# Kernel tuning notes

Hardware: AMD Instinct MI355X
Metric: run time of the kernel (lower is better)

The kernel has to match this reference:

```python
import jax, jax.numpy as jnp
import numpy as np

TEMP = 0.07
GAMMA1 = 0.8
GAMMA2 = 0.8
TAU = 0.1
BETA = 40.0
NUM_CT = 5
EPS = float(np.finfo(np.float32).eps)


def setup_inputs() -> dict:
    key = jax.random.key(0)
    ks = jax.random.split(key, 12)
    B, D, N, Bc = 8192, 512, 1000000, 4096
    img = jax.random.normal(ks[0], (B, D), jnp.float32)
    txt = jax.random.normal(ks[1], (B, D), jnp.float32)
    # CLIP-style unit-norm features keep sim in [-1,1] so exp() stays stable
    img = img / jnp.linalg.norm(img, axis=1, keepdims=True)
    txt = txt / jnp.linalg.norm(txt, axis=1, keepdims=True)
    image_ids = jax.random.randint(ks[2], (B,), 0, N)
    text_ids = jax.random.randint(ks[3], (B,), 0, N)
    slabel = jax.random.randint(ks[4], (B,), 0, 2)
    img_feas_c = jax.random.normal(ks[5], (Bc, D), jnp.float32)
    img_feas_c = img_feas_c / jnp.linalg.norm(img_feas_c, axis=1, keepdims=True)
    txt_feas_c = jax.random.normal(ks[6], (NUM_CT, D), jnp.float32)
    txt_feas_c = txt_feas_c / jnp.linalg.norm(txt_feas_c, axis=1, keepdims=True)
    labels_c = jax.random.randint(ks[7], (Bc,), 0, NUM_CT)
    last_loss_c = jax.random.uniform(ks[8], (Bc,), jnp.float32) * 2.0
    # persistent moving-average buffers (positive values, as they hold past exp-means)
    s_I = jax.random.uniform(ks[9], (N,), jnp.float32) + 0.5
    s_T = jax.random.uniform(ks[10], (N,), jnp.float32) + 0.5
    u = jnp.zeros((NUM_CT,), jnp.float32)
    return dict(image_features=img, text_features=txt, image_ids=image_ids,
                text_ids=text_ids, slabel=slabel, epoch=1,
                img_feas_c=img_feas_c, txt_feas_c=txt_feas_c, labels_c=labels_c,
                last_loss_c=last_loss_c, s_I=s_I, s_T=s_T, u=u)


def reference(image_features, text_features, image_ids, text_ids, slabel, epoch,
              img_feas_c, txt_feas_c, labels_c, last_loss_c, s_I, s_T, u):
    sg = jax.lax.stop_gradient
    # pairwise similarity GEMM  [B, B]
    sim = jnp.einsum('id,jd->ij', image_features, text_features)
    diag = jnp.diagonal(sim)
    pos = slabel == 1
    neg = ~pos
    pos_image_ids = image_ids[pos]
    pos_text_ids = text_ids[pos]
    # masked pairwise similarity differences: [P, B-P] and [B-P, P]
    image_diffs = (sim - diag[:, None])[pos][:, neg]
    text_diffs = (sim - diag[None, :])[neg][:, pos]
    image_diffs_d = sg(image_diffs / TEMP)
    text_diffs_d = sg(text_diffs / TEMP)
    exp_i = jnp.exp(image_diffs_d)
    exp_t = jnp.exp(text_diffs_d)
    g_I = jnp.mean(exp_i, axis=1, keepdims=True)   # [P, 1]
    g_T = jnp.mean(exp_t, axis=0, keepdims=True)   # [1, P]
    if epoch == 0:
        sI = g_I
        sT = g_T
    else:
        sI = ((1.0 - GAMMA1) * s_I[pos_image_ids] + GAMMA1 * g_I.squeeze()).reshape(g_I.shape)
        sT = ((1.0 - GAMMA1) * s_T[pos_text_ids] + GAMMA1 * g_T.squeeze()).reshape(g_T.shape)
    # persistent buffer scatter updates
    s_I_new = s_I.at[pos_image_ids].set(sI.squeeze())
    s_T_new = s_T.at[pos_text_ids].set(sT.squeeze())
    w_i = exp_i / (sI + EPS)
    w_t = exp_t / (sT + EPS)
    image_loss = jnp.mean(w_i * image_diffs, axis=1)
    text_loss = jnp.mean(w_t * text_diffs, axis=0)
    contrastive_loss = image_loss.mean() + text_loss.mean()
    # per-class CE penalty branch
    logits = (1.0 / TAU) * img_feas_c @ txt_feas_c.T           # [Bc, NUM_CT]
    logp = jax.nn.log_softmax(logits, axis=-1)
    ce = -logp[jnp.arange(logits.shape[0]), labels_c]          # [Bc]
    counts = jax.ops.segment_sum(jnp.ones_like(ce), labels_c, num_segments=NUM_CT)
    present = counts > 0
    safe_counts = jnp.maximum(counts, 1.0)
    mean_by_cls = jax.ops.segment_sum(ce, labels_c, num_segments=NUM_CT) / safe_counts
    mean_by_cls_last = jax.ops.segment_sum(last_loss_c, labels_c, num_segments=NUM_CT) / safe_counts
    cv = mean_by_cls - mean_by_cls_last
    u_sum = jnp.sum(jnp.where(present, u, 0.0))
    u_upd = jnp.where(u_sum == 0.0, sg(cv), (1.0 - GAMMA2) * u + GAMMA2 * sg(cv))
    u_new = jnp.where(present, u_upd, u)
    beta = BETA  # cosine=False
    cl = sg(jnp.maximum(beta * u_new, 0.0)) * mean_by_cls * TAU
    n_present = jnp.sum(present.astype(jnp.float32))
    constraint_mean = jnp.sum(jnp.where(present, cl, 0.0)) / n_present
    loss = contrastive_loss + constraint_mean
    return loss, s_I_new, s_T_new, u_new
```

## Files before the change

### kernel.cpp

```cpp
#include <hip/hip_runtime.h>

#define NBATCH 8192
#define DD 512
#define NIDS 1000000
#define BCNT 4096
#define NCT 5
#define INV_TEMP 14.285714285714286f
#define EPSF 1.1920929e-07f

typedef __attribute__((ext_vector_type(8))) short bf16x8;
typedef __attribute__((ext_vector_type(4))) float f32x4;
typedef __attribute__((ext_vector_type(8))) unsigned short u16x8;

#define OFF_LP     ((size_t)0)
#define OFF_CE1    ((size_t)1024)
#define OFF_CE2    ((size_t)2304)
#define OFF_CE3    ((size_t)3584)
#define OFF_POS    ((size_t)(32*1024))
#define OFF_RNK    ((size_t)(64*1024))
#define OFF_CNT    ((size_t)(96*1024))
#define OFF_DA     ((size_t)(100*1024))
#define OFF_RA0    ((size_t)(132*1024))
#define OFF_RB0    ((size_t)(164*1024))
#define OFF_RA1    ((size_t)(196*1024))
#define OFF_RB1    ((size_t)(228*1024))
#define OFF_SIV    ((size_t)(260*1024))
#define OFF_STV    ((size_t)(292*1024))
#define OFF_WINI   ((size_t)(324*1024))
#define OFF_WINT   (OFF_WINI + 4000000)
#define OFF_MA     (OFF_WINT + 4000000)
#define MATB       ((size_t)(8192*512*2))
#define OFF_MB     (OFF_MA + MATB)
#define OFF_MC     (OFF_MB + MATB)
#define OFF_MD     (OFF_MC + MATB)


__device__ __forceinline__ unsigned short f2bf(float x) {
    unsigned int u = __float_as_uint(x);
    unsigned int r = (u + 0x7fffu + ((u >> 16) & 1u)) >> 16;
    return (unsigned short)r;
}

__global__ __launch_bounds__(256) void k_pre(
        const float* __restrict__ sI, const float* __restrict__ sT,
        float* __restrict__ out, int* __restrict__ winI, int* __restrict__ winT,
        float* __restrict__ rA0, float* __restrict__ rB0,
        float* __restrict__ rA1, float* __restrict__ rB1,
        const int* __restrict__ slabel, int* __restrict__ pos,
        int* __restrict__ rnk, int* __restrict__ cnts,
        const float* __restrict__ imgc, const float* __restrict__ tfc,
        const int* __restrict__ labels, const float* __restrict__ lastl,
        float* __restrict__ ce1, float* __restrict__ ce2, float* __restrict__ ce3) {
    int bid = blockIdx.x;
    int tid = threadIdx.x;
    int iv = bid * 256 + tid;
    if (iv < NIDS) {
        out[1 + iv] = sI[iv];
        out[1 + NIDS + iv] = sT[iv];
        winI[iv] = -1;
        winT[iv] = -1;
    }
    if (iv < NBATCH) { rA0[iv] = 0.f; rB0[iv] = 0.f; rA1[iv] = 0.f; rB1[iv] = 0.f; }
    if (bid < 3907) return;

    if (bid == 3971) {
        __shared__ int sums[256];
        int base = tid * 32;
        int c = 0;
        for (int j = 0; j < 32; ++j) c += (slabel[base + j] == 1);
        sums[tid] = c;
        __syncthreads();
        for (int off = 1; off < 256; off <<= 1) {
            int add = (tid >= off) ? sums[tid - off] : 0;
            __syncthreads();
            sums[tid] += add;
            __syncthreads();
        }
        int p = sums[tid] - c;
        for (int j = 0; j < 32; ++j) {
            int idx = base + j;
            if (slabel[idx] == 1) { pos[p] = idx; rnk[idx] = p; p++; }
            else rnk[idx] = idx - p;
        }
        if (tid == 255) { cnts[0] = sums[255]; cnts[1] = NBATCH - sums[255]; }
    } else {
        int cb = bid - 3907;
        __shared__ float tS[NCT * DD];
        __shared__ float sce[NCT], scn[NCT], sls[NCT];
        for (int j = tid; j < NCT * DD; j += 256) tS[j] = tfc[j];
        if (tid < NCT) { sce[tid] = 0.f; scn[tid] = 0.f; sls[tid] = 0.f; }
        __syncthreads();
        int lane = tid & 63;
        int wid = tid >> 6;
        for (int it = 0; it < 16; ++it) {
            int r = it * 256 + cb * 4 + wid;
            const float4* ip = (const float4*)(imgc + (size_t)r * DD) + lane * 2;
            float4 a0 = ip[0], a1 = ip[1];
            float p[NCT];
#pragma unroll
            for (int c = 0; c < NCT; ++c) {
                const float* t = &tS[c * DD + lane * 8];
                p[c] = a0.x * t[0] + a0.y * t[1] + a0.z * t[2] + a0.w * t[3]
                     + a1.x * t[4] + a1.y * t[5] + a1.z * t[6] + a1.w * t[7];
            }
#pragma unroll
            for (int c = 0; c < NCT; ++c)
                for (int off = 32; off; off >>= 1) p[c] += __shfl_xor(p[c], off);
            if (lane == 0) {
                float l[NCT];
                float mx = -1e30f;
#pragma unroll
                for (int c = 0; c < NCT; ++c) { l[c] = p[c] * 10.0f; mx = fmaxf(mx, l[c]); }
                float ssum = 0.f;
#pragma unroll
                for (int c = 0; c < NCT; ++c) ssum += __expf(l[c] - mx);
                float lse = mx + __logf(ssum);
                int lb = labels[r];
                float ce = lse - l[lb];
                atomicAdd(&sce[lb], ce);
                atomicAdd(&scn[lb], 1.f);
                atomicAdd(&sls[lb], lastl[r]);
            }
        }
        __syncthreads();
        if (tid < NCT) {
            ce1[cb * 5 + tid] = sce[tid];
            ce2[cb * 5 + tid] = scn[tid];
            ce3[cb * 5 + tid] = sls[tid];
        }
    }
}

__global__ __launch_bounds__(256) void k_gather(
        const float* __restrict__ img, const float* __restrict__ txt,
        const int* __restrict__ slabel, const int* __restrict__ rnk,
        unsigned short* __restrict__ mA, unsigned short* __restrict__ mB,
        unsigned short* __restrict__ mC, unsigned short* __restrict__ mD,
        float* __restrict__ dA) {
    int tid = threadIdx.x;
    int i = blockIdx.x * 4 + (tid >> 6);
    int g = tid & 63;
    const float4* ip = (const float4*)(img + (size_t)i * DD) + g * 2;
    const float4* tp = (const float4*)(txt + (size_t)i * DD) + g * 2;
    float4 v0 = ip[0], v1 = ip[1], t0 = tp[0], t1 = tp[1];
    float part = v0.x * t0.x + v0.y * t0.y + v0.z * t0.z + v0.w * t0.w
               + v1.x * t1.x + v1.y * t1.y + v1.z * t1.z + v1.w * t1.w;
    for (int off = 32; off; off >>= 1) part += __shfl_xor(part, off);

    int lab = (slabel[i] == 1);
    int r = rnk[i];
    u16x8 oi, ot;
    oi[0] = f2bf(v0.x); oi[1] = f2bf(v0.y); oi[2] = f2bf(v0.z); oi[3] = f2bf(v0.w);
    oi[4] = f2bf(v1.x); oi[5] = f2bf(v1.y); oi[6] = f2bf(v1.z); oi[7] = f2bf(v1.w);
    ot[0] = f2bf(t0.x); ot[1] = f2bf(t0.y); ot[2] = f2bf(t0.z); ot[3] = f2bf(t0.w);
    ot[4] = f2bf(t1.x); ot[5] = f2bf(t1.y); ot[6] = f2bf(t1.z); ot[7] = f2bf(t1.w);

    int kc = g >> 2, gg = g & 3, rl = r & 127;
    int kb = (gg * 16) ^ ((rl & 6) << 3);
    size_t off = (size_t)(r >> 7) * 65536 + (size_t)kc * 4096 + rl * 32 + (kb >> 1);
    unsigned short* dI = lab ? mA : mD;
    unsigned short* dT = lab ? mC : mB;
    *(u16x8*)(dI + off) = oi;
    *(u16x8*)(dT + off) = ot;
    if (lab && g == 0) dA[r] = part;
}

__device__ __forceinline__ void gl16(const unsigned short* src, unsigned short* lds) {
    __builtin_amdgcn_global_load_lds((const __attribute__((address_space(1))) void*)src,
                                     (__attribute__((address_space(3))) void*)lds, 16, 0, 0);
}

#define VM4()  asm volatile("s_waitcnt vmcnt(4)" ::: "memory")
#define VM0()  asm volatile("s_waitcnt vmcnt(0)" ::: "memory")
#define BARR() asm volatile("s_barrier" ::: "memory")

__global__ __launch_bounds__(256) void k_gemm(
        const unsigned short* __restrict__ mA, const unsigned short* __restrict__ mB,
        const unsigned short* __restrict__ mC, const unsigned short* __restrict__ mD,
        const float* __restrict__ dA, const int* __restrict__ cnts,
        float* __restrict__ rA0, float* __restrict__ rB0,
        float* __restrict__ rA1, float* __restrict__ rB1) {
    int P = cnts[0], Nn = cnts[1];
    int bm = blockIdx.x * 128, bn = blockIdx.y * 128;
    if (bm >= P || bn >= Nn) return;
    int z = blockIdx.z;
    const unsigned short* Ap = (z ? mC : mA) + (size_t)blockIdx.x * 65536;
    const unsigned short* Bp = (z ? mD : mB) + (size_t)blockIdx.y * 65536;
    float* rA = z ? rA1 : rA0;
    float* rB = z ? rB1 : rB0;

    __shared__ __align__(16) char SRAW[36864];
    unsigned short* S0 = (unsigned short*)SRAW;

    int tid = threadIdx.x;
    int lane = tid & 63;
    int wid = tid >> 6;
    int wr = wid >> 1, wc = wid & 1;
    int soff = tid * 8;

    int kswz = ((lane >> 4) * 16) ^ ((lane & 6) << 3);
    int abyte = (wr * 64 + (lane & 15)) * 64 + kswz;
    int bbyte = (wc * 64 + (lane & 15)) * 64 + kswz;

    f32x4 acc[4][4];
#pragma unroll
    for (int m = 0; m < 4; ++m)
#pragma unroll
        for (int n = 0; n < 4; ++n) acc[m][n] = (f32x4){0.f, 0.f, 0.f, 0.f};

#define STAGE(kt, p) do { \
        gl16(Ap + (kt) * 4096 + soff,        S0 + (p) * 8192 + soff); \
        gl16(Ap + (kt) * 4096 + soff + 2048, S0 + (p) * 8192 + soff + 2048); \
        gl16(Bp + (kt) * 4096 + soff,        S0 + (p) * 8192 + 4096 + soff); \
        gl16(Bp + (kt) * 4096 + soff + 2048, S0 + (p) * 8192 + 4096 + soff + 2048); } while (0)

    STAGE(0, 0);
    STAGE(1, 1);
    VM4();
    BARR();

#pragma unroll
    for (int kt = 0; kt < 16; ++kt) {
        const int cur = kt & 1;
        bf16x8 af[4], bfv[4];
#pragma unroll
        for (int m = 0; m < 4; ++m)
            af[m] = *(const bf16x8*)((const char*)S0 + cur * 16384 + abyte + m * 1024);
#pragma unroll
        for (int n = 0; n < 4; ++n)
            bfv[n] = *(const bf16x8*)((const char*)S0 + cur * 16384 + 8192 + bbyte + n * 1024);
#pragma unroll
        for (int m = 0; m < 4; ++m)
#pragma unroll
            for (int n = 0; n < 4; ++n)
                acc[m][n] = __builtin_amdgcn_mfma_f32_16x16x32_bf16(af[m], bfv[n], acc[m][n], 0, 0, 0);
        if (kt < 15) {
            BARR();
            if (kt + 2 < 16) {
                STAGE(kt + 2, cur);
                VM4();
            } else {
                VM0();
            }
            BARR();
        }
    }
#undef STAGE

    BARR();
    float* F = (float*)SRAW;
    int col = lane & 15;
    int rsub = (lane >> 4) * 4;
    int rowbase = bm + wr * 64;
    int colb = bn + wc * 64 + col;
    int fb = ((wc << 7) + (wr << 6)) * 36 + col * 2;
#pragma unroll
    for (int m = 0; m < 4; ++m) {
#pragma unroll
        for (int r = 0; r < 4; ++r) {
            int wrow = m * 16 + rsub + r;
            float dv = dA[rowbase + wrow];
            float pa = 0.f, pb = 0.f;
#pragma unroll
            for (int n = 0; n < 4; ++n) {
                int gcol = colb + n * 16;
                float sv = acc[m][n][r];
                float df = sv - dv;
                float e = (gcol < Nn) ? __expf(df * INV_TEMP) : 0.f;
                pa += e;
                pb += e * df;
            }
            *(float2*)&F[fb + wrow * 36] = make_float2(pa, pb);
        }
    }
    BARR();
    {
        int row = tid >> 1;
        int half = tid & 1;
        const float4* Fr = (const float4*)&F[((half << 7) + row) * 36];
        float sa = 0.f, sb = 0.f;
#pragma unroll
        for (int q = 0; q < 8; ++q) {
            float4 v = Fr[q];
            sa += v.x + v.z;
            sb += v.y + v.w;
        }
        sa += __shfl_xor(sa, 1);
        sb += __shfl_xor(sb, 1);
        int grow = bm + row;
        if (!half && grow < P) {
            atomicAdd(&rA[grow], sa);
            atomicAdd(&rB[grow], sb);
        }
    }
}

__global__ void k_posfin(const int* __restrict__ cnts, const int* __restrict__ pos,
                         const float* __restrict__ rA0, const float* __restrict__ rB0,
                         const float* __restrict__ rA1, const float* __restrict__ rB1,
                         const int* __restrict__ image_ids, const int* __restrict__ text_ids,
                         const float* __restrict__ sIin, const float* __restrict__ sTin,
                         const int* __restrict__ epochp,
                         float* __restrict__ sIv, float* __restrict__ sTv,
                         int* __restrict__ winI, int* __restrict__ winT,
                         float* __restrict__ lp) {
    int k = blockIdx.x * 256 + threadIdx.x;
    int P = cnts[0], Nn = cnts[1];
    float invNn = 1.f / (float)Nn;
    int epoch = epochp[0];
    float lI = 0.f, lT = 0.f;
    if (k < P) {
        int i = pos[k];
        int idI = image_ids[i], idT = text_ids[i];
        float gI = rA0[k] * invNn;
        float sIvk = (epoch == 0) ? gI : 0.2f * sIin[idI] + 0.8f * gI;
        lI = (rB0[k] * invNn) / (sIvk + EPSF);
        float gT = rA1[k] * invNn;
        float sTvk = (epoch == 0) ? gT : 0.2f * sTin[idT] + 0.8f * gT;
        lT = (rB1[k] * invNn) / (sTvk + EPSF);
        sIv[k] = sIvk;
        sTv[k] = sTvk;
        atomicMax(&winI[idI], k);
        atomicMax(&winT[idT], k);
    }
    for (int off = 32; off; off >>= 1) { lI += __shfl_xor(lI, off); lT += __shfl_xor(lT, off); }
    if ((threadIdx.x & 63) == 0) {
        int slot = blockIdx.x * 4 + (threadIdx.x >> 6);
        lp[slot * 2] = lI;
        lp[slot * 2 + 1] = lT;
    }
}

__global__ void k_fin(const int* __restrict__ cnts, const int* __restrict__ pos,
                      const int* __restrict__ image_ids, const int* __restrict__ text_ids,
                      const int* __restrict__ winI, const int* __restrict__ winT,
                      const float* __restrict__ sIv, const float* __restrict__ sTv,
                      const float* __restrict__ lp, const float* __restrict__ ce1,
                      const float* __restrict__ ce2, const float* __restrict__ ce3,
                      const float* __restrict__ u, float* __restrict__ out) {
    int P = cnts[0];
    int k = blockIdx.x * 256 + threadIdx.x;
    if (k < P) {
        int i = pos[k];
        int a = image_ids[i];
        if (winI[a] == k) out[1 + a] = sIv[k];
        int b = text_ids[i];
        if (winT[b] == k) out[1 + NIDS + b] = sTv[k];
    }
    if (blockIdx.x == 0 && threadIdx.x < 64) {
        int lane = threadIdx.x;
        float lI = lp[2 * lane] + lp[2 * (lane + 64)];
        float lT = lp[2 * lane + 1] + lp[2 * (lane + 64) + 1];
        for (int off = 32; off; off >>= 1) { lI += __shfl_xor(lI, off); lT += __shfl_xor(lT, off); }
        float ce[NCT], cn[NCT], ls[NCT];
#pragma unroll
        for (int c = 0; c < NCT; ++c) {
            float a1 = ce1[lane * 5 + c], a2 = ce2[lane * 5 + c], a3 = ce3[lane * 5 + c];
            for (int off = 32; off; off >>= 1) {
                a1 += __shfl_xor(a1, off);
                a2 += __shfl_xor(a2, off);
                a3 += __shfl_xor(a3, off);
            }
            ce[c] = a1; cn[c] = a2; ls[c] = a3;
        }
        if (lane == 0) {
            float Pf = (float)P;
            float contrast = lI / Pf + lT / Pf;
            float u_sum = 0.f;
            float mc[NCT], cv[NCT], u_new[NCT];
            bool pres[NCT];
#pragma unroll
            for (int c = 0; c < NCT; ++c) {
                pres[c] = cn[c] > 0.f;
                float safe = fmaxf(cn[c], 1.f);
                mc[c] = ce[c] / safe;
                float ml = ls[c] / safe;
                cv[c] = mc[c] - ml;
                if (pres[c]) u_sum += u[c];
            }
            float np_ = 0.f, csum = 0.f;
#pragma unroll
            for (int c = 0; c < NCT; ++c) {
                float uu = (u_sum == 0.f) ? cv[c] : 0.2f * u[c] + 0.8f * cv[c];
                u_new[c] = pres[c] ? uu : u[c];
                if (pres[c]) {
                    np_ += 1.f;
                    csum += fmaxf(40.0f * u_new[c], 0.f) * mc[c] * 0.1f;
                }
                out[1 + 2 * NIDS + c] = u_new[c];
            }
            out[0] = contrast + csum / np_;
        }
    }
}

extern "C" void kernel_launch(void* const* d_in, const int* in_sizes, int n_in,
                              void* d_out, int out_size, void* d_ws, size_t ws_size,
                              hipStream_t stream) {
    const float* img = (const float*)d_in[0];
    const float* txt = (const float*)d_in[1];
    const int* image_ids = (const int*)d_in[2];
    const int* text_ids = (const int*)d_in[3];
    const int* slabel = (const int*)d_in[4];
    const int* epoch = (const int*)d_in[5];
    const float* imgc = (const float*)d_in[6];
    const float* tfc = (const float*)d_in[7];
    const int* labels = (const int*)d_in[8];
    const float* lastl = (const float*)d_in[9];
    const float* sI = (const float*)d_in[10];
    const float* sT = (const float*)d_in[11];
    const float* u = (const float*)d_in[12];
    float* out = (float*)d_out;
    char* ws = (char*)d_ws;

    float* lp = (float*)(ws + OFF_LP);
    float* ce1 = (float*)(ws + OFF_CE1);
    float* ce2 = (float*)(ws + OFF_CE2);
    float* ce3 = (float*)(ws + OFF_CE3);
    int* pos = (int*)(ws + OFF_POS);
    int* rnk = (int*)(ws + OFF_RNK);
    int* cnts = (int*)(ws + OFF_CNT);
    float* dA = (float*)(ws + OFF_DA);
    float* rA0 = (float*)(ws + OFF_RA0);
    float* rB0 = (float*)(ws + OFF_RB0);
    float* rA1 = (float*)(ws + OFF_RA1);
    float* rB1 = (float*)(ws + OFF_RB1);
    float* sIv = (float*)(ws + OFF_SIV);
    float* sTv = (float*)(ws + OFF_STV);
    int* winI = (int*)(ws + OFF_WINI);
    int* winT = (int*)(ws + OFF_WINT);
    unsigned short* mA = (unsigned short*)(ws + OFF_MA);
    unsigned short* mB = (unsigned short*)(ws + OFF_MB);
    unsigned short* mC = (unsigned short*)(ws + OFF_MC);
    unsigned short* mD = (unsigned short*)(ws + OFF_MD);

    k_pre<<<3972, 256, 0, stream>>>(sI, sT, out, winI, winT, rA0, rB0, rA1, rB1,
                                    slabel, pos, rnk, cnts,
                                    imgc, tfc, labels, lastl, ce1, ce2, ce3);
    k_gather<<<2048, 256, 0, stream>>>(img, txt, slabel, rnk, mA, mB, mC, mD, dA);
    k_gemm<<<dim3(64, 64, 2), 256, 0, stream>>>(mA, mB, mC, mD, dA, cnts, rA0, rB0, rA1, rB1);
    k_posfin<<<32, 256, 0, stream>>>(cnts, pos, rA0, rB0, rA1, rB1, image_ids, text_ids,
                                     sI, sT, epoch, sIv, sTv, winI, winT, lp);
    k_fin<<<32, 256, 0, stream>>>(cnts, pos, image_ids, text_ids, winI, winT,
                                  sIv, sTv, lp, ce1, ce2, ce3, u, out);
}
```

Before: 87.98 us.

## Widen GEMM block tile to 128x256 so each A tile is reused across two B tiles

The similarity GEMM block tile grows from 128x128 to 128x256. Each block now stages one A panel and two B panels per k-step, each wave computes a 64x128 sub-tile (32 accumulators), and the grid halves in y. The aim is to cut redundant A loads and LDS traffic per MFMA and to amortize barriers. In exchange it doubles the accumulator registers, raises LDS use to 48KB, and halves the number of blocks, which may reduce occupancy or leave some CUs idle.

After: 92.73 us. 5.4% more time.

```diff
diff --git a/kernel.cpp b/kernel.cpp
--- a/kernel.cpp
+++ b/kernel.cpp
@@ -170,26 +170,29 @@
                                      (__attribute__((address_space(3))) void*)lds, 16, 0, 0);
 }
 
-#define VM4()  asm volatile("s_waitcnt vmcnt(4)" ::: "memory")
+#define VM6()  asm volatile("s_waitcnt vmcnt(6)" ::: "memory")
 #define VM0()  asm volatile("s_waitcnt vmcnt(0)" ::: "memory")
+#define LGK0() asm volatile("s_waitcnt lgkmcnt(0)" ::: "memory")
 #define BARR() asm volatile("s_barrier" ::: "memory")
 
-__global__ __launch_bounds__(256) void k_gemm(
+__global__ __launch_bounds__(256, 2) void k_gemm(
         const unsigned short* __restrict__ mA, const unsigned short* __restrict__ mB,
         const unsigned short* __restrict__ mC, const unsigned short* __restrict__ mD,
         const float* __restrict__ dA, const int* __restrict__ cnts,
         float* __restrict__ rA0, float* __restrict__ rB0,
         float* __restrict__ rA1, float* __restrict__ rB1) {
     int P = cnts[0], Nn = cnts[1];
-    int bm = blockIdx.x * 128, bn = blockIdx.y * 128;
+    int bm = blockIdx.x * 128, bn = blockIdx.y * 256;
     if (bm >= P || bn >= Nn) return;
     int z = blockIdx.z;
     const unsigned short* Ap = (z ? mC : mA) + (size_t)blockIdx.x * 65536;
-    const unsigned short* Bp = (z ? mD : mB) + (size_t)blockIdx.y * 65536;
+    const unsigned short* Bp0 = (z ? mD : mB) + (size_t)(blockIdx.y * 2) * 65536;
+    const unsigned short* Bp1 = Bp0 + 65536;
+
     float* rA = z ? rA1 : rA0;
     float* rB = z ? rB1 : rB0;
 
-    __shared__ __align__(16) char SRAW[36864];
+    __shared__ __align__(16) char SRAW[49152];
     unsigned short* S0 = (unsigned short*)SRAW;
 
     int tid = threadIdx.x;
@@ -200,45 +203,57 @@
 
     int kswz = ((lane >> 4) * 16) ^ ((lane & 6) << 3);
     int abyte = (wr * 64 + (lane & 15)) * 64 + kswz;
-    int bbyte = (wc * 64 + (lane & 15)) * 64 + kswz;
-
-    f32x4 acc[4][4];
+    int bbyte = (lane & 15) * 64 + kswz;
+    int bregion = 8192 + wc * 8192;
+
+    f32x4 acc[4][8];
 #pragma unroll
     for (int m = 0; m < 4; ++m)
 #pragma unroll
-        for (int n = 0; n < 4; ++n) acc[m][n] = (f32x4){0.f, 0.f, 0.f, 0.f};
+        for (int n = 0; n < 8; ++n) acc[m][n] = (f32x4){0.f, 0.f, 0.f, 0.f};
 
 #define STAGE(kt, p) do { \
-        gl16(Ap + (kt) * 4096 + soff,        S0 + (p) * 8192 + soff); \
-        gl16(Ap + (kt) * 4096 + soff + 2048, S0 + (p) * 8192 + soff + 2048); \
-        gl16(Bp + (kt) * 4096 + soff,        S0 + (p) * 8192 + 4096 + soff); \
-        gl16(Bp + (kt) * 4096 + soff + 2048, S0 + (p) * 8192 + 4096 + soff + 2048); } while (0)
+        gl16(Ap + (kt) * 4096 + soff,         S0 + (p) * 12288 + soff); \
+        gl16(Ap + (kt) * 4096 + soff + 2048,  S0 + (p) * 12288 + soff + 2048); \
+        gl16(Bp0 + (kt) * 4096 + soff,        S0 + (p) * 12288 + 4096 + soff); \
+        gl16(Bp0 + (kt) * 4096 + soff + 2048, S0 + (p) * 12288 + 4096 + soff + 2048); \
+        gl16(Bp1 + (kt) * 4096 + soff,        S0 + (p) * 12288 + 8192 + soff); \
+        gl16(Bp1 + (kt) * 4096 + soff + 2048, S0 + (p) * 12288 + 8192 + soff + 2048); } while (0)
 
     STAGE(0, 0);
     STAGE(1, 1);
-    VM4();
+    VM6();
     BARR();
 
 #pragma unroll
     for (int kt = 0; kt < 16; ++kt) {
         const int cur = kt & 1;
-        bf16x8 af[4], bfv[4];
+        const char* base = (const char*)S0 + cur * 24576;
+        bf16x8 af[4], bfa[4], bfb[4];
 #pragma unroll
         for (int m = 0; m < 4; ++m)
-            af[m] = *(const bf16x8*)((const char*)S0 + cur * 16384 + abyte + m * 1024);
+            af[m] = *(const bf16x8*)(base + abyte + m * 1024);
 #pragma unroll
         for (int n = 0; n < 4; ++n)
-            bfv[n] = *(const bf16x8*)((const char*)S0 + cur * 16384 + 8192 + bbyte + n * 1024);
+            bfa[n] = *(const bf16x8*)(base + bregion + bbyte + n * 1024);
 #pragma unroll
         for (int m = 0; m < 4; ++m)
 #pragma unroll
             for (int n = 0; n < 4; ++n)
-                acc[m][n] = __builtin_amdgcn_mfma_f32_16x16x32_bf16(af[m], bfv[n], acc[m][n], 0, 0, 0);
+                acc[m][n] = __builtin_amdgcn_mfma_f32_16x16x32_bf16(af[m], bfa[n], acc[m][n], 0, 0, 0);
+#pragma unroll
+        for (int n = 0; n < 4; ++n)
+            bfb[n] = *(const bf16x8*)(base + bregion + bbyte + (n + 4) * 1024);
+#pragma unroll
+        for (int m = 0; m < 4; ++m)
+#pragma unroll
+            for (int n = 0; n < 4; ++n)
+                acc[m][n + 4] = __builtin_amdgcn_mfma_f32_16x16x32_bf16(af[m], bfb[n], acc[m][n + 4], 0, 0, 0);
         if (kt < 15) {
             BARR();
             if (kt + 2 < 16) {
                 STAGE(kt + 2, cur);
-                VM4();
+                VM6();
             } else {
                 VM0();
             }
@@ -252,7 +267,7 @@
     int col = lane & 15;
     int rsub = (lane >> 4) * 4;
     int rowbase = bm + wr * 64;
-    int colb = bn + wc * 64 + col;
+    int colb = bn + wc * 128 + col;
     int fb = ((wc << 7) + (wr << 6)) * 36 + col * 2;
 #pragma unroll
     for (int m = 0; m < 4; ++m) {
@@ -262,17 +277,20 @@
             float dv = dA[rowbase + wrow];
             float pa = 0.f, pb = 0.f;
 #pragma unroll
-            for (int n = 0; n < 4; ++n) {
+            for (int n = 0; n < 8; ++n) {
                 int gcol = colb + n * 16;
-                float sv = acc[m][n][r];
-                float df = sv - dv;
-                float e = (gcol < Nn) ? __expf(df * INV_TEMP) : 0.f;
-                pa += e;
-                pb += e * df;
+                if (gcol < Nn) {
+                    float sv = acc[m][n][r];
+                    float df = sv - dv;
+                    float e = __expf(df * INV_TEMP);
+                    pa += e;
+                    pb += e * df;
+                }
             }
             *(float2*)&F[fb + wrow * 36] = make_float2(pa, pb);
         }
     }
+    LGK0();
     BARR();
     {
         int row = tid >> 1;
@@ -438,7 +456,7 @@
                                     slabel, pos, rnk, cnts,
                                     imgc, tfc, labels, lastl, ce1, ce2, ce3);
     k_gather<<<2048, 256, 0, stream>>>(img, txt, slabel, rnk, mA, mB, mC, mD, dA);
-    k_gemm<<<dim3(64, 64, 2), 256, 0, stream>>>(mA, mB, mC, mD, dA, cnts, rA0, rB0, rA1, rB1);
+    k_gemm<<<dim3(64, 32, 2), 256, 0, stream>>>(mA, mB, mC, mD, dA, cnts, rA0, rB0, rA1, rB1);
     k_posfin<<<32, 256, 0, stream>>>(cnts, pos, rA0, rB0, rA1, rB1, image_ids, text_ids,
                                      sI, sT, epoch, sIv, sTv, winI, winT, lp);
     k_fin<<<32, 256, 0, stream>>>(cnts, pos, image_ids, text_ids, winI, winT,
```
